# Kernel tuning notes

Measured on AMD Instinct MI355X. Metric: run time of the kernel, lower is better.

Reference implementation:

```python
import jax, jax.numpy as jnp
import numpy as np

N, K, D = 500000, 16, 16


def setup_inputs() -> dict:
    key = jax.random.key(0)
    k1, k2, k3, k4 = jax.random.split(key, 4)
    x = jax.random.normal(k1, (N, D), dtype=jnp.float32)
    # mixture weights: positive, sum to 1, shape (1, K)
    pi = jax.nn.softmax(jax.random.normal(k2, (1, K), dtype=jnp.float32), axis=-1)
    mu = jax.random.normal(k3, (K, 1, D), dtype=jnp.float32)
    # SPD covariance per cluster: A A^T / D + I
    A = jax.random.normal(k4, (K, D, D), dtype=jnp.float32)
    Sigma = jnp.einsum('kde,kfe->kdf', A, A) / D + jnp.eye(D, dtype=jnp.float32)
    return {"x": x, "pi": pi, "mu": mu, "Sigma": Sigma}


def reference(x, pi, mu, Sigma):
    # Batched MultivariateNormal log_prob over K clusters (replaces the
    # Python loop over torch.distributions.MultivariateNormal).
    d = x.shape[-1]
    L = jnp.linalg.cholesky(Sigma)                      # (K, D, D)
    diff = x[None, :, :] - mu                           # (K, N, D) via mu (K,1,D)
    # solve L y = diff^T per cluster -> Mahalanobis = ||y||^2
    y = jax.vmap(lambda Lk, dk: jax.scipy.linalg.solve_triangular(Lk, dk.T, lower=True))(L, diff)  # (K, D, N)
    maha = jnp.sum(y * y, axis=1)                       # (K, N)
    half_logdet = jnp.sum(jnp.log(jnp.diagonal(L, axis1=-2, axis2=-1)), axis=-1)  # (K,)
    log2pi = jnp.log(jnp.asarray(2.0 * np.pi, dtype=x.dtype))
    logp = -0.5 * (maha + d * log2pi) - half_logdet[:, None]  # (K, N)
    res_k = jnp.exp(logp).T * pi                        # (N, K), pi broadcasts from (1,K)
    res = res_k / jnp.sum(res_k, axis=1, keepdims=True)  # (N, K)
    return res
```

## Files before the change

### kernel.cpp

```cpp
#include <hip/hip_runtime.h>
#include <math.h>

#define D 16
#define K 16
#define BLK 256

#define OFF_A 0
#define OFF_T 2048
#define OFF_C 2304

typedef _Float16 f16x8 __attribute__((ext_vector_type(8)));
typedef float    f32x16 __attribute__((ext_vector_type(16)));
typedef _Float16 h2 __attribute__((ext_vector_type(2)));

__host__ __device__ constexpr int tri(int i, int j) { return i * (i + 1) / 2 + j; }

static __device__ __forceinline__ unsigned pack2(float f0, float f1) {
    _Float16 h0 = (_Float16)f0, h1 = (_Float16)f1;
    unsigned short b0 = __builtin_bit_cast(unsigned short, h0);
    unsigned short b1 = __builtin_bit_cast(unsigned short, h1);
    return ((unsigned)b1 << 16) | (unsigned)b0;
}

__global__ __launch_bounds__(64) void gmm_prep(
    const float* __restrict__ pi, const float* __restrict__ mu,
    const float* __restrict__ Sigma, float* __restrict__ P)
{
    const int k = threadIdx.x;
    if (k >= K) return;

    float M[tri(D - 1, D - 1) + 1];

#pragma unroll
    for (int i = 0; i < D; ++i)
#pragma unroll
        for (int j = 0; j <= i; ++j)
            M[tri(i, j)] = Sigma[k * D * D + i * D + j];

    float invd[D];
    float prod = 1.f;
#pragma unroll
    for (int j = 0; j < D; ++j) {
        float s = M[tri(j, j)];
#pragma unroll
        for (int p = 0; p < j; ++p) s -= M[tri(j, p)] * M[tri(j, p)];
        float ljj = sqrtf(s);
        prod *= ljj;
        float inv = 1.f / ljj;
        invd[j] = inv;
        M[tri(j, j)] = ljj;
#pragma unroll
        for (int i = j + 1; i < D; ++i) {
            float t = M[tri(i, j)];
#pragma unroll
            for (int p = 0; p < j; ++p) t -= M[tri(i, p)] * M[tri(j, p)];
            M[tri(i, j)] = t * inv;
        }
    }

#pragma unroll
    for (int j = 0; j < D; ++j) {
        M[tri(j, j)] = invd[j];
#pragma unroll
        for (int i = j + 1; i < D; ++i) {
            float s = 0.f;
#pragma unroll
            for (int p = j; p < i; ++p) s += M[tri(i, p)] * M[tri(p, j)];
            M[tri(i, j)] = -s * invd[i];
        }
    }

    const float invs2 = 0.70710678118654752440f;

    float t[D];
#pragma unroll
    for (int i = 0; i < D; ++i) {
        float acc = 0.f;
#pragma unroll
        for (int j = 0; j <= i; ++j) acc += M[tri(i, j)] * mu[k * D + j];
        t[i] = acc * invs2;
    }

    P[OFF_C + k] = logf(pi[k] / prod);

    const int tt = k >> 1;
    const int hi = (k & 1) * 8;
#pragma unroll
    for (int w = 0; w < 2; ++w)
#pragma unroll
        for (int ii = 0; ii < 8; ++ii) {
            int comp = (ii & 3) + 8 * (ii >> 2) + 4 * w;
            P[OFF_T + tt * 32 + w * 16 + hi + ii] = -t[comp];
        }

    uint4* PA = (uint4*)(P + OFF_A);
#pragma unroll
    for (int mm = 0; mm < 32; ++mm) {
        int m  = (k & 1) * 16 + (mm & 15) + 32 * (mm >> 4);
        int rr = m & 15;
        int kc = (m >> 5) * 8;
        unsigned dw[4];
#pragma unroll
        for (int e = 0; e < 4; ++e) {
            int c0 = kc + 2 * e, c1 = c0 + 1;
            float f0 = (c0 <= rr) ? M[tri(rr, c0)] * invs2 : 0.f;
            float f1 = (c1 <= rr) ? M[tri(rr, c1)] * invs2 : 0.f;
            dw[e] = pack2(f0, f1);
        }
        PA[tt * 64 + m] = make_uint4(dw[0], dw[1], dw[2], dw[3]);
    }
}

__global__ __launch_bounds__(BLK) void gmm_main(
    const float* __restrict__ x, const float* __restrict__ P,
    float* __restrict__ out, int N)
{
    const int tid  = threadIdx.x;
    const int lane = tid & 63;
    const int wave = tid >> 6;
    const int cc   = lane & 31;
    const int w    = lane >> 5;
    const long long n = (long long)blockIdx.x * BLK + tid;
    const bool ok = n < (long long)N;

    __shared__ __align__(16) unsigned short xs[4][64][24];
    __shared__ __align__(64) float ts[256];

    f16x8 Afr[8];
#pragma unroll
    for (int t = 0; t < 8; ++t)
        Afr[t] = ((const f16x8*)(P + OFF_A))[t * 64 + lane];

    if (tid < 64) ((float4*)ts)[tid] = ((const float4*)(P + OFF_T))[tid];

    float4 xr0 = {0, 0, 0, 0}, xr1 = xr0, xr2 = xr0, xr3 = xr0;
    if (ok) {
        const float4* p = (const float4*)(x + n * D);
        xr0 = p[0]; xr1 = p[1]; xr2 = p[2]; xr3 = p[3];
    }
    h2 xp[8];
    xp[0] = (h2){(_Float16)xr0.x, (_Float16)xr0.y};
    xp[1] = (h2){(_Float16)xr0.z, (_Float16)xr0.w};
    xp[2] = (h2){(_Float16)xr1.x, (_Float16)xr1.y};
    xp[3] = (h2){(_Float16)xr1.z, (_Float16)xr1.w};
    xp[4] = (h2){(_Float16)xr2.x, (_Float16)xr2.y};
    xp[5] = (h2){(_Float16)xr2.z, (_Float16)xr2.w};
    xp[6] = (h2){(_Float16)xr3.x, (_Float16)xr3.y};
    xp[7] = (h2){(_Float16)xr3.z, (_Float16)xr3.w};

    uint4* rowq = (uint4*)&xs[wave][lane][0];
    rowq[0] = make_uint4(__builtin_bit_cast(unsigned, xp[0]),
                         __builtin_bit_cast(unsigned, xp[1]),
                         __builtin_bit_cast(unsigned, xp[2]),
                         __builtin_bit_cast(unsigned, xp[3]));
    rowq[1] = make_uint4(__builtin_bit_cast(unsigned, xp[4]),
                         __builtin_bit_cast(unsigned, xp[5]),
                         __builtin_bit_cast(unsigned, xp[6]),
                         __builtin_bit_cast(unsigned, xp[7]));

    __syncthreads();

    f16x8 Bfr[2];
#pragma unroll
    for (int ct = 0; ct < 2; ++ct)
        Bfr[ct] = *(const f16x8*)(&xs[wave][ct * 32 + cc][w * 8]);

    float r[K];
#pragma unroll
    for (int t = 0; t < 8; ++t) {
        f32x16 ci = *(const f32x16*)(&ts[t * 32 + w * 16]);
#pragma unroll
        for (int ct = 0; ct < 2; ++ct) {
            f32x16 a = __builtin_amdgcn_mfma_f32_32x32x16_f16(
                Afr[t], Bfr[ct], ci, 0, 0, 0);
            float q0 = fmaf(a[0], a[0], a[1] * a[1]);
            float q1 = fmaf(a[2], a[2], a[3] * a[3]);
            float q2 = fmaf(a[4], a[4], a[5] * a[5]);
            float q3 = fmaf(a[6], a[6], a[7] * a[7]);
            float pA = (q0 + q1) + (q2 + q3);
            float q4 = fmaf(a[8],  a[8],  a[9]  * a[9]);
            float q5 = fmaf(a[10], a[10], a[11] * a[11]);
            float q6 = fmaf(a[12], a[12], a[13] * a[13]);
            float q7 = fmaf(a[14], a[14], a[15] * a[15]);
            float pB = (q4 + q5) + (q6 + q7);
            pA += __shfl_xor(pA, 32);
            pB += __shfl_xor(pB, 32);
            if (ct == w) { r[2 * t] = pA; r[2 * t + 1] = pB; }
        }
    }

    const float* __restrict__ Pc = P + OFF_C;
#pragma unroll
    for (int kk = 0; kk < K; ++kk) r[kk] = Pc[kk] - r[kk];

    float mx = r[0];
#pragma unroll
    for (int kk = 1; kk < K; ++kk) mx = fmaxf(mx, r[kk]);
    float sum = 0.f;
#pragma unroll
    for (int kk = 0; kk < K; ++kk) {
        float e = __expf(r[kk] - mx);
        r[kk] = e;
        sum += e;
    }
    float inv = 1.f / sum;
    if (ok) {
        float4* po = (float4*)(out + n * D);
        po[0] = (float4){r[0] * inv,  r[1] * inv,  r[2] * inv,  r[3] * inv};
        po[1] = (float4){r[4] * inv,  r[5] * inv,  r[6] * inv,  r[7] * inv};
        po[2] = (float4){r[8] * inv,  r[9] * inv,  r[10] * inv, r[11] * inv};
        po[3] = (float4){r[12] * inv, r[13] * inv, r[14] * inv, r[15] * inv};
    }
}

extern "C" void kernel_launch(void* const* d_in, const int* in_sizes, int n_in,
                              void* d_out, int out_size, void* d_ws, size_t ws_size,
                              hipStream_t stream) {
    const float* x     = (const float*)d_in[0];
    const float* pi    = (const float*)d_in[1];
    const float* mu    = (const float*)d_in[2];
    const float* Sigma = (const float*)d_in[3];
    float* out = (float*)d_out;
    const int N = in_sizes[0] / D;

    float* P = (float*)d_ws;

    gmm_prep<<<1, 64, 0, stream>>>(pi, mu, Sigma, P);

    const int grid = (N + BLK - 1) / BLK;
    gmm_main<<<grid, BLK, 0, stream>>>(x, P, out, N);
}
```

Baseline: 104.2 us.

## Process two points per thread and use nontemporal loads and stores

Each block now handles 512 points instead of 256, with each thread loading and scoring two points. This spreads the per-block loading of A fragments and constants over twice as many points and puts more memory loads in flight per thread. Global loads of x and stores of the output now use nontemporal hints. In exchange the kernel uses more registers and twice the shared memory per block, and launches half as many blocks, which may lower occupancy.

```diff
diff --git a/kernel.cpp b/kernel.cpp
--- a/kernel.cpp
+++ b/kernel.cpp
@@ -4,6 +4,7 @@
 #define D 16
 #define K 16
 #define BLK 256
+#define PPB 512
 
 #define OFF_A 0
 #define OFF_T 2048
@@ -11,6 +12,7 @@
 
 typedef _Float16 f16x8 __attribute__((ext_vector_type(8)));
 typedef float    f32x16 __attribute__((ext_vector_type(16)));
+typedef float    f32x4  __attribute__((ext_vector_type(4)));
 typedef _Float16 h2 __attribute__((ext_vector_type(2)));
 
 __host__ __device__ constexpr int tri(int i, int j) { return i * (i + 1) / 2 + j; }
@@ -120,10 +122,12 @@
     const int wave = tid >> 6;
     const int cc   = lane & 31;
     const int w    = lane >> 5;
-    const long long n = (long long)blockIdx.x * BLK + tid;
-    const bool ok = n < (long long)N;
-
-    __shared__ __align__(16) unsigned short xs[4][64][24];
+    const long long n0 = (long long)blockIdx.x * PPB + tid;
+    const long long n1 = n0 + BLK;
+    const bool ok0 = n0 < (long long)N;
+    const bool ok1 = n1 < (long long)N;
+
+    __shared__ __align__(16) unsigned short xs[4][128][24];
     __shared__ __align__(64) float ts[256];
 
     f16x8 Afr[8];
@@ -133,44 +137,52 @@
 
     if (tid < 64) ((float4*)ts)[tid] = ((const float4*)(P + OFF_T))[tid];
 
-    float4 xr0 = {0, 0, 0, 0}, xr1 = xr0, xr2 = xr0, xr3 = xr0;
-    if (ok) {
-        const float4* p = (const float4*)(x + n * D);
-        xr0 = p[0]; xr1 = p[1]; xr2 = p[2]; xr3 = p[3];
-    }
-    h2 xp[8];
-    xp[0] = (h2){(_Float16)xr0.x, (_Float16)xr0.y};
-    xp[1] = (h2){(_Float16)xr0.z, (_Float16)xr0.w};
-    xp[2] = (h2){(_Float16)xr1.x, (_Float16)xr1.y};
-    xp[3] = (h2){(_Float16)xr1.z, (_Float16)xr1.w};
-    xp[4] = (h2){(_Float16)xr2.x, (_Float16)xr2.y};
-    xp[5] = (h2){(_Float16)xr2.z, (_Float16)xr2.w};
-    xp[6] = (h2){(_Float16)xr3.x, (_Float16)xr3.y};
-    xp[7] = (h2){(_Float16)xr3.z, (_Float16)xr3.w};
-
-    uint4* rowq = (uint4*)&xs[wave][lane][0];
-    rowq[0] = make_uint4(__builtin_bit_cast(unsigned, xp[0]),
-                         __builtin_bit_cast(unsigned, xp[1]),
-                         __builtin_bit_cast(unsigned, xp[2]),
-                         __builtin_bit_cast(unsigned, xp[3]));
-    rowq[1] = make_uint4(__builtin_bit_cast(unsigned, xp[4]),
-                         __builtin_bit_cast(unsigned, xp[5]),
-                         __builtin_bit_cast(unsigned, xp[6]),
-                         __builtin_bit_cast(unsigned, xp[7]));
+    f32x4 xr[8];
+#pragma unroll
+    for (int q = 0; q < 8; ++q) xr[q] = (f32x4){0.f, 0.f, 0.f, 0.f};
+    if (ok0) {
+        const f32x4* p = (const f32x4*)(x + n0 * D);
+#pragma unroll
+        for (int q = 0; q < 4; ++q) xr[q] = __builtin_nontemporal_load(p + q);
+    }
+    if (ok1) {
+        const f32x4* p = (const f32x4*)(x + n1 * D);
+#pragma unroll
+        for (int q = 0; q < 4; ++q) xr[4 + q] = __builtin_nontemporal_load(p + q);
+    }
+
+#pragma unroll
+    for (int g = 0; g < 2; ++g) {
+        h2 xp[8];
+#pragma unroll
+        for (int q = 0; q < 4; ++q) {
+            xp[2 * q]     = (h2){(_Float16)xr[4 * g + q].x, (_Float16)xr[4 * g + q].y};
+            xp[2 * q + 1] = (h2){(_Float16)xr[4 * g + q].z, (_Float16)xr[4 * g + q].w};
+        }
+        uint4* rowq = (uint4*)&xs[wave][g * 64 + lane][0];
+        rowq[0] = make_uint4(__builtin_bit_cast(unsigned, xp[0]),
+                             __builtin_bit_cast(unsigned, xp[1]),
+                             __builtin_bit_cast(unsigned, xp[2]),
+                             __builtin_bit_cast(unsigned, xp[3]));
+        rowq[1] = make_uint4(__builtin_bit_cast(unsigned, xp[4]),
+                             __builtin_bit_cast(unsigned, xp[5]),
+                             __builtin_bit_cast(unsigned, xp[6]),
+                             __builtin_bit_cast(unsigned, xp[7]));
+    }
 
     __syncthreads();
 
-    f16x8 Bfr[2];
-#pragma unroll
-    for (int ct = 0; ct < 2; ++ct)
+    f16x8 Bfr[4];
+#pragma unroll
+    for (int ct = 0; ct < 4; ++ct)
         Bfr[ct] = *(const f16x8*)(&xs[wave][ct * 32 + cc][w * 8]);
 
-    float r[K];
+    float r0[K], r1[K];
 #pragma unroll
     for (int t = 0; t < 8; ++t) {
         f32x16 ci = *(const f32x16*)(&ts[t * 32 + w * 16]);
 #pragma unroll
-        for (int ct = 0; ct < 2; ++ct) {
+        for (int ct = 0; ct < 4; ++ct) {
             f32x16 a = __builtin_amdgcn_mfma_f32_32x32x16_f16(
                 Afr[t], Bfr[ct], ci, 0, 0, 0);
             float q0 = fmaf(a[0], a[0], a[1] * a[1]);
@@ -185,31 +197,50 @@
             float pB = (q4 + q5) + (q6 + q7);
             pA += __shfl_xor(pA, 32);
             pB += __shfl_xor(pB, 32);
-            if (ct == w) { r[2 * t] = pA; r[2 * t + 1] = pB; }
+            if (ct == w)     { r0[2 * t] = pA; r0[2 * t + 1] = pB; }
+            if (ct == w + 2) { r1[2 * t] = pA; r1[2 * t + 1] = pB; }
         }
     }
 
     const float* __restrict__ Pc = P + OFF_C;
 #pragma unroll
-    for (int kk = 0; kk < K; ++kk) r[kk] = Pc[kk] - r[kk];
-
-    float mx = r[0];
-#pragma unroll
-    for (int kk = 1; kk < K; ++kk) mx = fmaxf(mx, r[kk]);
-    float sum = 0.f;
-#pragma unroll
-    for (int kk = 0; kk < K; ++kk) {
-        float e = __expf(r[kk] - mx);
-        r[kk] = e;
-        sum += e;
-    }
-    float inv = 1.f / sum;
-    if (ok) {
-        float4* po = (float4*)(out + n * D);
-        po[0] = (float4){r[0] * inv,  r[1] * inv,  r[2] * inv,  r[3] * inv};
-        po[1] = (float4){r[4] * inv,  r[5] * inv,  r[6] * inv,  r[7] * inv};
-        po[2] = (float4){r[8] * inv,  r[9] * inv,  r[10] * inv, r[11] * inv};
-        po[3] = (float4){r[12] * inv, r[13] * inv, r[14] * inv, r[15] * inv};
+    for (int kk = 0; kk < K; ++kk) { r0[kk] = Pc[kk] - r0[kk]; r1[kk] = Pc[kk] - r1[kk]; }
+
+    {
+        float mx = r0[0];
+#pragma unroll
+        for (int kk = 1; kk < K; ++kk) mx = fmaxf(mx, r0[kk]);
+        float sum = 0.f;
+#pragma unroll
+        for (int kk = 0; kk < K; ++kk) { float e = __expf(r0[kk] - mx); r0[kk] = e; sum += e; }
+        float inv = 1.f / sum;
+        if (ok0) {
+            f32x4* po = (f32x4*)(out + n0 * D);
+#pragma unroll
+            for (int q = 0; q < 4; ++q) {
+                f32x4 v = {r0[4 * q] * inv, r0[4 * q + 1] * inv,
+                           r0[4 * q + 2] * inv, r0[4 * q + 3] * inv};
+                __builtin_nontemporal_store(v, po + q);
+            }
+        }
+    }
+    {
+        float mx = r1[0];
+#pragma unroll
+        for (int kk = 1; kk < K; ++kk) mx = fmaxf(mx, r1[kk]);
+        float sum = 0.f;
+#pragma unroll
+        for (int kk = 0; kk < K; ++kk) { float e = __expf(r1[kk] - mx); r1[kk] = e; sum += e; }
+        float inv = 1.f / sum;
+        if (ok1) {
+            f32x4* po = (f32x4*)(out + n1 * D);
+#pragma unroll
+            for (int q = 0; q < 4; ++q) {
+                f32x4 v = {r1[4 * q] * inv, r1[4 * q + 1] * inv,
+                           r1[4 * q + 2] * inv, r1[4 * q + 3] * inv};
+                __builtin_nontemporal_store(v, po + q);
+            }
+        }
     }
 }
 
@@ -227,6 +258,6 @@
 
     gmm_prep<<<1, 64, 0, stream>>>(pi, mu, Sigma, P);
 
-    const int grid = (N + BLK - 1) / BLK;
+    const int grid = (N + PPB - 1) / PPB;
     gmm_main<<<grid, BLK, 0, stream>>>(x, P, out, N);
 }
```

Result: slower. 127.1 us (+22.0%).
